# Optimization experiments

Measured on AMD Instinct MI355X. Metric: run time of the kernel, lower is better.

The kernel has to match this reference:

```python
import jax, jax.numpy as jnp
import numpy as np

EDGES = [(5, 7), (7, 9), (6, 8), (8, 10), (5, 6), (5, 11), (6, 12), (11, 12),
         (11, 13), (13, 15), (12, 14), (14, 16), (0, 5), (0, 6)]
N_NODES = 17

def _build_norm_adj():
    # aggregated[dst] += h[src] for both directions; then divide by clamped in-degree.
    A = np.zeros((N_NODES, N_NODES), dtype=np.float32)
    for s, d in EDGES:
        A[d, s] += 1.0
        A[s, d] += 1.0
    deg = np.clip(A.sum(axis=1, keepdims=True), 1.0, None)
    return jnp.asarray(A / deg)  # (17, 17)

_A_NORM = _build_norm_adj()

def _bn17(x, gamma, beta, eps=1e-5):
    # BatchNorm1d(17) on (B, 17, D): stats over batch and feature dims per node channel.
    mean = x.mean(axis=(0, 2), keepdims=True)
    var = x.var(axis=(0, 2), keepdims=True)  # biased, matching torch training mode
    return gamma[None, :, None] * (x - mean) * jax.lax.rsqrt(var + eps) + beta[None, :, None]

def setup_inputs() -> dict:
    key = jax.random.key(0)
    ks = jax.random.split(key, 8)
    B, H, E = 65536, 64, 128
    s = 0.1
    return {
        "x": jax.random.normal(ks[0], (B, N_NODES, 2), jnp.float32),
        "W_enc": jax.random.normal(ks[1], (2, H), jnp.float32) * s,
        "b_enc": jnp.zeros((H,), jnp.float32),
        "W_gc1": jax.random.normal(ks[2], (H, H), jnp.float32) * s,
        "b_gc1": jnp.zeros((H,), jnp.float32),
        "W_gc2": jax.random.normal(ks[3], (H, H), jnp.float32) * s,
        "b_gc2": jnp.zeros((H,), jnp.float32),
        "gamma1": jnp.ones((N_NODES,), jnp.float32),
        "beta1": jnp.zeros((N_NODES,), jnp.float32),
        "gamma2": jnp.ones((N_NODES,), jnp.float32),
        "beta2": jnp.zeros((N_NODES,), jnp.float32),
        "W_p1": jax.random.normal(ks[4], (N_NODES * H, 256), jnp.float32) * s,
        "b_p1": jnp.zeros((256,), jnp.float32),
        "W_p2": jax.random.normal(ks[5], (256, E), jnp.float32) * s,
        "b_p2": jnp.zeros((E,), jnp.float32),
    }

def reference(x, W_enc, b_enc, W_gc1, b_gc1, W_gc2, b_gc2,
              gamma1, beta1, gamma2, beta2, W_p1, b_p1, W_p2, b_p2):
    B = x.shape[0]
    # node encoder (dropout = identity at inference)
    h = jax.nn.relu(jnp.einsum('bnc,cd->bnd', x, W_enc) + b_enc)
    # graph conv 1: normalized neighbor mean via fixed adjacency
    h_agg = jnp.einsum('ij,bjd->bid', _A_NORM, h)
    h = _bn17(h + h_agg, gamma1, beta1)
    h = jax.nn.relu(jnp.einsum('bnd,de->bne', h, W_gc1) + b_gc1)
    # graph conv 2
    h_agg = jnp.einsum('ij,bjd->bid', _A_NORM, h)
    h = _bn17(h + h_agg, gamma2, beta2)
    h = jax.nn.relu(jnp.einsum('bnd,de->bne', h, W_gc2) + b_gc2)
    # pool MLP (dropout = identity)
    pooled = h.reshape(B, -1)  # (B, 17*64)
    z = jax.nn.relu(pooled @ W_p1 + b_p1)
    emb = z @ W_p2 + b_p2
    # L2 normalize (torch F.normalize eps=1e-12)
    norm = jnp.sqrt(jnp.sum(emb * emb, axis=1, keepdims=True))
    return emb / jnp.maximum(norm, 1e-12)
```

## Files before the change

kernel.cpp:

```cpp
#include <hip/hip_runtime.h>
#include <hip/hip_bf16.h>

typedef unsigned int  uint32;
typedef unsigned short ushort16;

#define B_TOTAL 65536
#define NN 17

typedef __bf16 bf16x8 __attribute__((ext_vector_type(8)));
typedef float  f32x4  __attribute__((ext_vector_type(4)));

static constexpr int   CNT[NN]    = {2,0,0,0,0,4,4,2,2,1,1,3,3,2,2,1,1};
static constexpr int   NBR[NN][4] = {
  {5,6,0,0},{0,0,0,0},{0,0,0,0},{0,0,0,0},{0,0,0,0},
  {7,6,11,0},{8,5,12,0},{5,9,0,0},{6,10,0,0},{7,0,0,0},{8,0,0,0},
  {5,12,13,0},{6,11,14,0},{11,15,0,0},{12,16,0,0},{13,0,0,0},{14,0,0,0}};
static constexpr float INVDEG[NN] = {0.5f,0.f,0.f,0.f,0.f,0.25f,0.25f,0.5f,0.5f,1.f,1.f,
  0.33333333333333333f,0.33333333333333333f,0.5f,0.5f,1.f,1.f};

#define S_BYTES   ((size_t)B_TOTAL * 1088 * 2)
#define STATS_OFF S_BYTES
#define W1_OFF    (STATS_OFF + 40960)
#define W2_OFF    (W1_OFF + (size_t)278528*2)
#define WGT_OFF   (W2_OFF + (size_t)65536)


__device__ inline ushort16 f2bfu(float f){
  union { __hip_bfloat16 h; ushort16 u; } c; c.h = __float2bfloat16(f); return c.u;
}

__device__ inline f32x4 MFMA(bf16x8 a, bf16x8 b, f32x4 c){
  return __builtin_amdgcn_mfma_f32_16x16x32_bf16(a, b, c, 0, 0, 0);
}

__device__ inline void gload_lds16(const void* g, void* l){
  __builtin_amdgcn_global_load_lds(
      (const __attribute__((address_space(1))) unsigned int*)g,
      (__attribute__((address_space(3))) unsigned int*)l, 16, 0, 0);
}

__device__ inline void enc_agg(const float* __restrict__ xb,
                               float we0, float we1, float be, float* s1){
  float h[NN];
  #pragma unroll
  for (int n = 0; n < NN; ++n)
    h[n] = fmaxf(fmaf(xb[2*n], we0, fmaf(xb[2*n+1], we1, be)), 0.f);
  #pragma unroll
  for (int n = 0; n < NN; ++n){
    float a = 0.f;
    #pragma unroll
    for (int j = 0; j < 4; ++j) if (j < CNT[n]) a += h[NBR[n][j]];
    s1[n] = fmaf(INVDEG[n], a, h[n]);
  }
}

__device__ inline void reduce_stats(float* sA, float* qA,
                                    float* __restrict__ gSum, float* __restrict__ gSq){
  int t = threadIdx.x;
  #pragma unroll
  for (int n = 0; n < NN; ++n){
    float s = sA[n], q = qA[n];
    #pragma unroll
    for (int off = 32; off > 0; off >>= 1){
      s += __shfl_down(s, off, 64);
      q += __shfl_down(q, off, 64);
    }
    sA[n] = s; qA[n] = q;
  }
  __shared__ float shS[NN], shQ[NN];
  if (t < NN){ shS[t] = 0.f; shQ[t] = 0.f; }
  __syncthreads();
  if ((t & 63) == 0){
    #pragma unroll
    for (int n = 0; n < NN; ++n){ atomicAdd(&shS[n], sA[n]); atomicAdd(&shQ[n], qA[n]); }
  }
  __syncthreads();
  if (t < NN){ atomicAdd(&gSum[t], shS[t]); atomicAdd(&gSq[t], shQ[t]); }
}

__device__ inline void mfma_stats(const char* hsm, float* sred, int t,
                                  float* __restrict__ gSum, float* __restrict__ gSq){
  const int w4 = t >> 6, lo = t & 15, q = (t >> 4) & 3;
  bf16x8 one;
  { union { ushort16 u[8]; bf16x8 v; } c;
    #pragma unroll
    for (int i = 0; i < 8; ++i) c.u[i] = 0x3F80;
    one = c.v; }
  #pragma unroll
  for (int i = 0; i < 5; ++i){
    int mt = w4 + i*4;
    if (mt < 17){
      f32x4 d0 = (f32x4)0.f, d1 = (f32x4)0.f;
      #pragma unroll
      for (int s = 0; s < 2; ++s){
        int r = mt*16 + lo;
        bf16x8 a = *(const bf16x8*)(hsm + ((r*128 + s*64 + q*16) ^ ((r & 7) << 4)));
        d0 = MFMA(a, one, d0);
        d1 = MFMA(a, a, d1);
      }
      if (lo == 0){
        #pragma unroll
        for (int j = 0; j < 4; ++j) sred[mt*16 + q*4 + j] = d0[j];
      }
      if ((lo >> 2) == q) sred[272 + mt*16 + lo] = d1[lo & 3];
    }
  }
  __syncthreads();
  if (t < NN){
    float s = 0.f, qq = 0.f;
    #pragma unroll
    for (int bl = 0; bl < 16; ++bl){
      s  += sred[t + 17*bl];
      qq += sred[272 + t + 17*bl];
    }
    atomicAdd(&gSum[t], s);
    atomicAdd(&gSq[t], qq);
  }
}

__global__ __launch_bounds__(256) void k_prep(const float* __restrict__ Wp1,
                                              const float* __restrict__ Wp2,
                                              const float* __restrict__ Wg1,
                                              const float* __restrict__ Wg2,
                                              ushort16* __restrict__ W1T,
                                              ushort16* __restrict__ W2T,
                                              ushort16* __restrict__ WGT,
                                              float* __restrict__ colsum2){
  int g = blockIdx.x * 256 + threadIdx.x;
  if (g < 278528){
    int n = g / 1088, k = g - n*1088;
    W1T[g] = f2bfu(Wp1[(size_t)k*256 + n]);
  } else if (g < 311296){
    int h = g - 278528;
    int e = h >> 8, k = h & 255;
    W2T[h] = f2bfu(Wp2[(size_t)k*128 + e]);
  } else if (g < 327680){
    int h = g - 311296;
    int sel = h >> 12;
    int idx = h & 4095;
    int e = idx >> 6, d = idx & 63;
    const float* Wsrc = (sel < 2) ? Wg1 : Wg2;
    float v = Wsrc[d*64 + e];
    __hip_bfloat16 hi = __float2bfloat16(v);
    if (sel & 1){
      float rem = v - __bfloat162float(hi);
      WGT[h] = f2bfu(rem);
    } else {
      WGT[h] = f2bfu(v);
    }
  } else {
    int e = g - 327680;
    if (e < 64){
      float cs = 0.f;
      for (int d = 0; d < 64; ++d){
        float v = Wg2[d*64 + e];
        float hi = __bfloat162float(__float2bfloat16(v));
        float lo = __bfloat162float(__float2bfloat16(v - hi));
        cs += hi + lo;
      }
      colsum2[e] = cs;
    }
  }
}

__global__ void k_sh(const float* __restrict__ shift2, const float* __restrict__ colsum2,
                     const float* __restrict__ bg2, float* __restrict__ SH){
  int n = blockIdx.x, e = threadIdx.x;
  SH[n*64 + e] = fmaf(shift2[n], colsum2[e], bg2[e]);
}

__global__ __launch_bounds__(256,4) void k_stats1(const float* __restrict__ x,
    const float* __restrict__ W_enc, const float* __restrict__ b_enc,
    float* __restrict__ gSum, float* __restrict__ gSq){
  __shared__ __align__(16) float xs[1088];
  int t = threadIdx.x, e = t & 63, lb = t >> 6;
  float we0 = W_enc[e], we1 = W_enc[64 + e], be = b_enc[e];
  const float4* xg = (const float4*)(x + (size_t)blockIdx.x*1088);
  ((float4*)xs)[t] = xg[t];
  if (t < 16) ((float4*)xs)[256 + t] = xg[256 + t];
  float sA[NN], qA[NN];
  #pragma unroll
  for (int n = 0; n < NN; ++n){ sA[n] = 0.f; qA[n] = 0.f; }
  __syncthreads();
  for (int it = 0; it < 8; ++it){
    float s1[NN];
    enc_agg(xs + (it*4 + lb)*34, we0, we1, be, s1);
    #pragma unroll
    for (int n = 0; n < NN; ++n){ sA[n] += s1[n]; qA[n] += s1[n]*s1[n]; }
  }
  int slot = (blockIdx.x & 31) * 32;
  reduce_stats(sA, qA, gSum + slot, gSq + slot);
}

__global__ void k_finalize(const float* __restrict__ gSum, const float* __restrict__ gSq,
                           const float* __restrict__ gamma, const float* __restrict__ beta,
                           float* __restrict__ scale, float* __restrict__ shift){
  int n = threadIdx.x;
  if (n < NN){
    float s = 0.f, qq = 0.f;
    for (int sl = 0; sl < 32; ++sl){ s += gSum[sl*32 + n]; qq += gSq[sl*32 + n]; }
    const float invC = 1.0f / (float)((size_t)B_TOTAL * 64);
    float mean = s * invC;
    float var  = qq * invC - mean*mean;
    float istd = rsqrtf(var + 1e-5f);
    float sc   = gamma[n] * istd;
    scale[n] = sc;
    shift[n] = fmaf(-mean, sc, beta[n]);
  }
}

__global__ __launch_bounds__(256,4) void k_gc1(const float* __restrict__ x,
    const float* __restrict__ W_enc, const float* __restrict__ b_enc,
    const float* __restrict__ bg,
    const float* __restrict__ scale, const float* __restrict__ shift,
    const __hip_bfloat16* __restrict__ Whi, const __hip_bfloat16* __restrict__ Wlo,
    __hip_bfloat16* __restrict__ S, float* __restrict__ gSum, float* __restrict__ gSq){
  __shared__ __align__(16) char hsm[272*128];
  __shared__ float sred[544];
  __shared__ __align__(16) float xs[544];
  __shared__ float sc_s[NN], sf_s[NN];
  const int t = threadIdx.x, e = t & 63, lb = t >> 6;
  const int w4 = t >> 6, lo = t & 15, q = (t >> 4) & 3;
  if (t < NN){ sc_s[t] = scale[t]; sf_s[t] = shift[t]; }
  if (t < 136) ((float4*)xs)[t] = ((const float4*)(x + (size_t)blockIdx.x*544))[t];
  float we0 = W_enc[e], we1 = W_enc[64 + e], be = b_enc[e];
  __syncthreads();

  for (int it = 0; it < 4; ++it){
    int bl = it*4 + lb;
    float s1[NN];
    enc_agg(xs + bl*34, we0, we1, be, s1);
    #pragma unroll
    for (int n = 0; n < NN; ++n){
      int row = bl*17 + n;
      int byt = (row*128 + 2*e) ^ ((row & 7) << 4);
      *(__hip_bfloat16*)(hsm + byt) = __float2bfloat16(fmaf(s1[n], sc_s[n], sf_s[n]));
    }
  }
  __syncthreads();

  const char* WhiB = (const char*)Whi;
  const char* WloB = (const char*)Wlo;
  f32x4 acc[5][4];
  #pragma unroll
  for (int i = 0; i < 5; ++i)
    #pragma unroll
    for (int et = 0; et < 4; ++et) acc[i][et] = (f32x4)0.f;
  #pragma unroll
  for (int et = 0; et < 4; ++et){
    int col = et*16 + lo;
    bf16x8 wh0 = *(const bf16x8*)(WhiB + col*128 +      q*16);
    bf16x8 wh1 = *(const bf16x8*)(WhiB + col*128 + 64 + q*16);
    bf16x8 wl0 = *(const bf16x8*)(WloB + col*128 +      q*16);
    bf16x8 wl1 = *(const bf16x8*)(WloB + col*128 + 64 + q*16);
    #pragma unroll
    for (int i = 0; i < 5; ++i){
      int mt = w4 + i*4;
      if (mt < 17){
        int r = mt*16 + lo;
        int base = r*128, sw = (r & 7) << 4;
        bf16x8 a0 = *(const bf16x8*)(hsm + ((base +      q*16) ^ sw));
        bf16x8 a1 = *(const bf16x8*)(hsm + ((base + 64 + q*16) ^ sw));
        acc[i][et] = MFMA(a0, wh0, acc[i][et]);
        acc[i][et] = MFMA(a1, wh1, acc[i][et]);
        acc[i][et] = MFMA(a0, wl0, acc[i][et]);
        acc[i][et] = MFMA(a1, wl1, acc[i][et]);
      }
    }
  }
  float bgv[4];
  #pragma unroll
  for (int et = 0; et < 4; ++et) bgv[et] = bg[et*16 + lo];
  __syncthreads();

  #pragma unroll
  for (int i = 0; i < 5; ++i){
    int mt = w4 + i*4;
    if (mt < 17){
      #pragma unroll
      for (int et = 0; et < 4; ++et){
        #pragma unroll
        for (int j = 0; j < 4; ++j){
          int row = mt*16 + q*4 + j;
          float h2 = fmaxf(acc[i][et][j] + bgv[et], 0.f);
          int byt = (row*128 + (et*16 + lo)*2) ^ ((row & 7) << 4);
          *(__hip_bfloat16*)(hsm + byt) = __float2bfloat16(h2);
        }
      }
    }
  }
  __syncthreads();

  for (int it = 0; it < 4; ++it){
    int bl = it*4 + lb;
    int row0 = bl*17;
    float h2v[NN];
    #pragma unroll
    for (int n = 0; n < NN; ++n){
      int row = row0 + n;
      h2v[n] = __bfloat162float(*(const __hip_bfloat16*)(hsm + ((row*128 + 2*e) ^ ((row & 7) << 4))));
    }
    #pragma unroll
    for (int n = 0; n < NN; ++n){
      float agg = 0.f;
      #pragma unroll
      for (int j = 0; j < 4; ++j) if (j < CNT[n]) agg += h2v[NBR[n][j]];
      float s2 = fmaf(INVDEG[n], agg, h2v[n]);
      int row = row0 + n;
      *(__hip_bfloat16*)(hsm + ((row*128 + 2*e) ^ ((row & 7) << 4))) = __float2bfloat16(s2);
    }
  }
  __syncthreads();

  int slot = (blockIdx.x & 31) * 32;
  mfma_stats(hsm, sred, t, gSum + slot, gSq + slot);

  const size_t gbase = (size_t)blockIdx.x * 34816;
  char* Sc = (char*)S;
  #pragma unroll
  for (int k = 0; k < 9; ++k){
    int g = t + k*256;
    if (g < 2176){
      int row = g >> 3;
      uint4 v = *(const uint4*)(hsm + ((g*16) ^ ((row & 7) << 4)));
      *(uint4*)(Sc + gbase + (size_t)g*16) = v;
    }
  }
}

__global__ __launch_bounds__(256,2) void k_back(
    const __hip_bfloat16* __restrict__ S,
    const ushort16* __restrict__ W1T, const float* __restrict__ b_p1,
    const ushort16* __restrict__ W2T, const float* __restrict__ b_p2,
    const __hip_bfloat16* __restrict__ WG2,
    const float* __restrict__ scale2, const float* __restrict__ SH,
    float* __restrict__ out){
  __shared__ __align__(16) char smem[65536];
  const int t = threadIdx.x;
  const int L = t & 63, w = t >> 6;
  const int lo = L & 15, q = L >> 4;
  const int wsw = ((lo >> 1) & 3) << 4;
  const size_t b0 = (size_t)blockIdx.x * 128;
  const char* Sb  = (const char*)S;
  const char* W1b = (const char*)W1T;
  const char* W2b = (const char*)W2T;
  const char* Wgb = (const char*)WG2;

  f32x4 acc[16][2];
  #pragma unroll
  for (int nt = 0; nt < 16; ++nt){ acc[nt][0] = (f32x4)0.f; acc[nt][1] = (f32x4)0.f; }

  bf16x8 wg[4][4];
  #pragma unroll
  for (int et = 0; et < 4; ++et){
    const char* A = Wgb + (et*16 + lo)*128 + q*16;
    wg[et][0] = *(const bf16x8*)(A);
    wg[et][1] = *(const bf16x8*)(A + 64);
    wg[et][2] = *(const bf16x8*)(A + 8192);
    wg[et][3] = *(const bf16x8*)(A + 8192 + 64);
  }

  const int csw = (((t & 3) * 16) ^ (((t >> 3) & 3) << 4));
  auto stageW = [&](int ks, int buf){
    size_t kb = (size_t)ks * 64;
    char* ldsbase = smem + 32768 + buf*16384 + w*1024;
    gload_lds16(W1b + (size_t)((  0 + t) >> 2)*2176 + kb + csw, ldsbase);
    gload_lds16(W1b + (size_t)((256 + t) >> 2)*2176 + kb + csw, ldsbase + 4096);
    gload_lds16(W1b + (size_t)((512 + t) >> 2)*2176 + kb + csw, ldsbase + 8192);
    gload_lds16(W1b + (size_t)((768 + t) >> 2)*2176 + kb + csw, ldsbase + 12288);
  };

  uint4 br[4];
  auto loadS2 = [&](int n){
    const char* base = Sb + (b0 + (size_t)(w*32 + lo))*2176 + n*128 + q*16;
    br[0] = *(const uint4*)(base);
    br[1] = *(const uint4*)(base + 64);
    br[2] = *(const uint4*)(base + 16*2176);
    br[3] = *(const uint4*)(base + 16*2176 + 64);
  };
  auto gc2w = [&](int n){
    char* Pb = smem + (n & 1)*16384;
    float sc = scale2[n];
    #pragma unroll
    for (int bt = 0; bt < 2; ++bt){
      f32x4 g[4];
      #pragma unroll
      for (int et = 0; et < 4; ++et) g[et] = (f32x4)0.f;
      union { uint4 u; bf16x8 v; } c0, c1;
      c0.u = br[bt*2]; c1.u = br[bt*2 + 1];
      #pragma unroll
      for (int et = 0; et < 4; ++et){
        g[et] = MFMA(wg[et][0], c0.v, g[et]);
        g[et] = MFMA(wg[et][2], c0.v, g[et]);
        g[et] = MFMA(wg[et][1], c1.v, g[et]);
        g[et] = MFMA(wg[et][3], c1.v, g[et]);
      }
      int b = w*32 + bt*16 + lo;
      #pragma unroll
      for (int et = 0; et < 4; ++et){
        float4 sh4 = *(const float4*)&SH[n*64 + et*16 + q*4];
        float v0 = fmaxf(fmaf(sc, g[et].x, sh4.x), 0.f);
        float v1 = fmaxf(fmaf(sc, g[et].y, sh4.y), 0.f);
        float v2 = fmaxf(fmaf(sc, g[et].z, sh4.z), 0.f);
        float v3 = fmaxf(fmaf(sc, g[et].w, sh4.w), 0.f);
        uint32 u0 = (uint32)f2bfu(v0) | ((uint32)f2bfu(v1) << 16);
        uint32 u1 = (uint32)f2bfu(v2) | ((uint32)f2bfu(v3) << 16);
        int byt = (b*128 + (et*16 + q*4)*2) ^ ((b & 7) << 4);
        *(uint2*)(Pb + byt) = make_uint2(u0, u1);
      }
    }
  };

  loadS2(0);
  gc2w(0);
  stageW(0, 0);
  __syncthreads();

  #pragma unroll 1
  for (int ks = 0; ks < 34; ++ks){
    const int cur = ks & 1, n = ks >> 1, half = ks & 1;
    if (ks < 33) stageW(ks + 1, cur ^ 1);
    if (half == 0 && n < 16) loadS2(n + 1);
    const char* Pb = smem + (n & 1)*16384;
    const char* Wb = smem + 32768 + (cur ? 16384 : 0);
    int r0 = w*32 + lo, r1 = w*32 + 16 + lo;
    bf16x8 pf0 = *(const bf16x8*)(Pb + ((r0*128 + half*64 + q*16) ^ ((r0 & 7) << 4)));
    bf16x8 pf1 = *(const bf16x8*)(Pb + ((r1*128 + half*64 + q*16) ^ ((r1 & 7) << 4)));
    #pragma unroll
    for (int nt = 0; nt < 16; ++nt){
      bf16x8 wf = *(const bf16x8*)(Wb + (nt*16 + lo)*64 + (q*16 ^ wsw));
      acc[nt][0] = MFMA(wf, pf0, acc[nt][0]);
      acc[nt][1] = MFMA(wf, pf1, acc[nt][1]);
    }
    if (half == 1 && n < 16) gc2w(n + 1);
    __syncthreads();
  }

  #pragma unroll
  for (int nt = 0; nt < 16; ++nt){
    float4 bias = *(const float4*)&b_p1[nt*16 + q*4];
    #pragma unroll
    for (int bt = 0; bt < 2; ++bt){
      int b = w*32 + bt*16 + lo;
      f32x4 v = acc[nt][bt];
      float z0 = fmaxf(v.x + bias.x, 0.f), z1 = fmaxf(v.y + bias.y, 0.f);
      float z2 = fmaxf(v.z + bias.z, 0.f), z3 = fmaxf(v.w + bias.w, 0.f);
      uint32 lo32 = (uint32)f2bfu(z0) | ((uint32)f2bfu(z1) << 16);
      uint32 hi32 = (uint32)f2bfu(z2) | ((uint32)f2bfu(z3) << 16);
      int nbyte = (nt*16 + q*4) * 2;
      int addr = b*512 + (nbyte ^ ((b & 7) << 4));
      *(uint2*)(smem + addr) = make_uint2(lo32, hi32);
    }
  }
  __syncthreads();

  f32x4 acc2[8][2];
  #pragma unroll
  for (int et = 0; et < 8; ++et){ acc2[et][0] = (f32x4)0.f; acc2[et][1] = (f32x4)0.f; }
  #pragma unroll 1
  for (int ks = 0; ks < 8; ++ks){
    bf16x8 zf0, zf1;
    {
      int b = w*32 + lo;
      int kb = ks*64 + q*16;
      zf0 = *(const bf16x8*)(smem + b*512 + (kb ^ ((b & 7) << 4)));
      b = w*32 + 16 + lo;
      zf1 = *(const bf16x8*)(smem + b*512 + (kb ^ ((b & 7) << 4)));
    }
    #pragma unroll
    for (int et = 0; et < 8; ++et){
      bf16x8 wf = *(const bf16x8*)(W2b + (et*16 + lo)*512 + ks*64 + q*16);
      acc2[et][0] = MFMA(wf, zf0, acc2[et][0]);
      acc2[et][1] = MFMA(wf, zf1, acc2[et][1]);
    }
  }

  #pragma unroll
  for (int bt = 0; bt < 2; ++bt){
    int b = w*32 + bt*16 + lo;
    float4 vv[8];
    float ss = 0.f;
    #pragma unroll
    for (int et = 0; et < 8; ++et){
      float4 bias = *(const float4*)&b_p2[et*16 + q*4];
      f32x4 a = bt ? acc2[et][1] : acc2[et][0];
      vv[et].x = a.x + bias.x; vv[et].y = a.y + bias.y;
      vv[et].z = a.z + bias.z; vv[et].w = a.w + bias.w;
      ss += vv[et].x*vv[et].x + vv[et].y*vv[et].y + vv[et].z*vv[et].z + vv[et].w*vv[et].w;
    }
    ss += __shfl_xor(ss, 16, 64);
    ss += __shfl_xor(ss, 32, 64);
    float inv = 1.0f / fmaxf(sqrtf(ss), 1e-12f);
    float* op = out + (b0 + b)*128;
    #pragma unroll
    for (int et = 0; et < 8; ++et){
      float4 o; o.x = vv[et].x*inv; o.y = vv[et].y*inv; o.z = vv[et].z*inv; o.w = vv[et].w*inv;
      *(float4*)(op + et*16 + q*4) = o;
    }
  }
}

extern "C" void kernel_launch(void* const* d_in, const int* in_sizes, int n_in,
                              void* d_out, int out_size, void* d_ws, size_t ws_size,
                              hipStream_t stream) {
  const float* x     = (const float*)d_in[0];
  const float* W_enc = (const float*)d_in[1];
  const float* b_enc = (const float*)d_in[2];
  const float* W_gc1 = (const float*)d_in[3];
  const float* b_gc1 = (const float*)d_in[4];
  const float* W_gc2 = (const float*)d_in[5];
  const float* b_gc2 = (const float*)d_in[6];
  const float* gamma1= (const float*)d_in[7];
  const float* beta1 = (const float*)d_in[8];
  const float* gamma2= (const float*)d_in[9];
  const float* beta2 = (const float*)d_in[10];
  const float* W_p1  = (const float*)d_in[11];
  const float* b_p1  = (const float*)d_in[12];
  const float* W_p2  = (const float*)d_in[13];
  const float* b_p2  = (const float*)d_in[14];
  float* out = (float*)d_out;

  char* ws = (char*)d_ws;
  __hip_bfloat16* S = (__hip_bfloat16*)ws;
  float*    stats = (float*)(ws + STATS_OFF);
  ushort16* W1T   = (ushort16*)(ws + W1_OFF);
  ushort16* W2T   = (ushort16*)(ws + W2_OFF);
  __hip_bfloat16* WGT = (__hip_bfloat16*)(ws + WGT_OFF);

  (void)hipMemsetAsync(stats, 0, 16384, stream);

  k_prep<<<1281, 256, 0, stream>>>(W_p1, W_p2, W_gc1, W_gc2, W1T, W2T,
                                   (ushort16*)WGT, stats + 4224);
  k_stats1<<<2048, 256, 0, stream>>>(x, W_enc, b_enc, stats + 0, stats + 1024);
  k_finalize<<<1, 32, 0, stream>>>(stats + 0, stats + 1024, gamma1, beta1,
                                   stats + 4096, stats + 4128);
  k_gc1<<<4096, 256, 0, stream>>>(x, W_enc, b_enc, b_gc1,
                                  stats + 4096, stats + 4128,
                                  WGT, WGT + 4096,
                                  S, stats + 2048, stats + 3072);
  k_finalize<<<1, 32, 0, stream>>>(stats + 2048, stats + 3072, gamma2, beta2,
                                   stats + 4160, stats + 4192);
  k_sh<<<17, 64, 0, stream>>>(stats + 4192, stats + 4224, b_gc2, stats + 4288);
  k_back<<<512, 256, 0, stream>>>(S, W1T, b_p1, W2T, b_p2,
                                  WGT + 8192, stats + 4160, stats + 4288, out);
}
```

Measured before the change: 325.9 us.

## Fuse second-layer aggregation, BN stats and store into one vectorized pass

The end of k_gc1 changes. Before, it did the neighbor aggregation per element, then a barrier, an MFMA-based stats pass and a separate copy-out. Now each thread takes a 16-byte octet of a row, reads the neighbor octets from LDS through a packed lookup table, computes the aggregate, writes the bf16 result straight to global memory, and accumulates sum and sum-of-squares with shuffles and LDS atomics. This removes one LDS round trip, two barriers and the MFMA stats, at the cost of more LDS atomics, a loop that is no longer unrolled, and integer-division arithmetic per slot. enc_agg also now reads the input as float2.

```diff
diff --git a/kernel.cpp b/kernel.cpp
--- a/kernel.cpp
+++ b/kernel.cpp
@@ -39,12 +39,19 @@
       (__attribute__((address_space(3))) unsigned int*)l, 16, 0, 0);
 }
 
-__device__ inline void enc_agg(const float* __restrict__ xb,
+__device__ inline void w8(uint4 u, float* f){
+  f[0]=__uint_as_float(u.x<<16); f[1]=__uint_as_float(u.x&0xFFFF0000u);
+  f[2]=__uint_as_float(u.y<<16); f[3]=__uint_as_float(u.y&0xFFFF0000u);
+  f[4]=__uint_as_float(u.z<<16); f[5]=__uint_as_float(u.z&0xFFFF0000u);
+  f[6]=__uint_as_float(u.w<<16); f[7]=__uint_as_float(u.w&0xFFFF0000u);
+}
+
+__device__ inline void enc_agg(const float2* __restrict__ xb,
                                float we0, float we1, float be, float* s1){
   float h[NN];
   #pragma unroll
   for (int n = 0; n < NN; ++n)
-    h[n] = fmaxf(fmaf(xb[2*n], we0, fmaf(xb[2*n+1], we1, be)), 0.f);
+    h[n] = fmaxf(fmaf(xb[n].x, we0, fmaf(xb[n].y, we1, be)), 0.f);
   #pragma unroll
   for (int n = 0; n < NN; ++n){
     float a = 0.f;
@@ -76,46 +83,6 @@
   }
   __syncthreads();
   if (t < NN){ atomicAdd(&gSum[t], shS[t]); atomicAdd(&gSq[t], shQ[t]); }
-}
-
-__device__ inline void mfma_stats(const char* hsm, float* sred, int t,
-                                  float* __restrict__ gSum, float* __restrict__ gSq){
-  const int w4 = t >> 6, lo = t & 15, q = (t >> 4) & 3;
-  bf16x8 one;
-  { union { ushort16 u[8]; bf16x8 v; } c;
-    #pragma unroll
-    for (int i = 0; i < 8; ++i) c.u[i] = 0x3F80;
-    one = c.v; }
-  #pragma unroll
-  for (int i = 0; i < 5; ++i){
-    int mt = w4 + i*4;
-    if (mt < 17){
-      f32x4 d0 = (f32x4)0.f, d1 = (f32x4)0.f;
-      #pragma unroll
-      for (int s = 0; s < 2; ++s){
-        int r = mt*16 + lo;
-        bf16x8 a = *(const bf16x8*)(hsm + ((r*128 + s*64 + q*16) ^ ((r & 7) << 4)));
-        d0 = MFMA(a, one, d0);
-        d1 = MFMA(a, a, d1);
-      }
-      if (lo == 0){
-        #pragma unroll
-        for (int j = 0; j < 4; ++j) sred[mt*16 + q*4 + j] = d0[j];
-      }
-      if ((lo >> 2) == q) sred[272 + mt*16 + lo] = d1[lo & 3];
-    }
-  }
-  __syncthreads();
-  if (t < NN){
-    float s = 0.f, qq = 0.f;
-    #pragma unroll
-    for (int bl = 0; bl < 16; ++bl){
-      s  += sred[t + 17*bl];
-      qq += sred[272 + t + 17*bl];
-    }
-    atomicAdd(&gSum[t], s);
-    atomicAdd(&gSq[t], qq);
-  }
 }
 
 __global__ __launch_bounds__(256) void k_prep(const float* __restrict__ Wp1,
@@ -184,7 +151,7 @@
   __syncthreads();
   for (int it = 0; it < 8; ++it){
     float s1[NN];
-    enc_agg(xs + (it*4 + lb)*34, we0, we1, be, s1);
+    enc_agg((const float2*)(xs + (it*4 + lb)*34), we0, we1, be, s1);
     #pragma unroll
     for (int n = 0; n < NN; ++n){ sA[n] += s1[n]; qA[n] += s1[n]*s1[n]; }
   }
@@ -216,12 +183,19 @@
     const __hip_bfloat16* __restrict__ Whi, const __hip_bfloat16* __restrict__ Wlo,
     __hip_bfloat16* __restrict__ S, float* __restrict__ gSum, float* __restrict__ gSq){
   __shared__ __align__(16) char hsm[272*128];
-  __shared__ float sred[544];
   __shared__ __align__(16) float xs[544];
   __shared__ float sc_s[NN], sf_s[NN];
+  __shared__ uint32 lutP[NN];
+  __shared__ float lutI[NN], shS[NN], shQ[NN];
   const int t = threadIdx.x, e = t & 63, lb = t >> 6;
   const int w4 = t >> 6, lo = t & 15, q = (t >> 4) & 3;
-  if (t < NN){ sc_s[t] = scale[t]; sf_s[t] = shift[t]; }
+  if (t < NN){
+    sc_s[t] = scale[t]; sf_s[t] = shift[t];
+    lutP[t] = (uint32)CNT[t] | ((uint32)NBR[t][0]<<3) | ((uint32)NBR[t][1]<<8)
+            | ((uint32)NBR[t][2]<<13) | ((uint32)NBR[t][3]<<18);
+    lutI[t] = INVDEG[t];
+    shS[t] = 0.f; shQ[t] = 0.f;
+  }
   if (t < 136) ((float4*)xs)[t] = ((const float4*)(x + (size_t)blockIdx.x*544))[t];
   float we0 = W_enc[e], we1 = W_enc[64 + e], be = b_enc[e];
   __syncthreads();
@@ -229,7 +203,7 @@
   for (int it = 0; it < 4; ++it){
     int bl = it*4 + lb;
     float s1[NN];
-    enc_agg(xs + bl*34, we0, we1, be, s1);
+    enc_agg((const float2*)(xs + bl*34), we0, we1, be, s1);
     #pragma unroll
     for (int n = 0; n < NN; ++n){
       int row = bl*17 + n;
@@ -291,40 +265,56 @@
   }
   __syncthreads();
 
-  for (int it = 0; it < 4; ++it){
-    int bl = it*4 + lb;
-    int row0 = bl*17;
-    float h2v[NN];
-    #pragma unroll
-    for (int n = 0; n < NN; ++n){
-      int row = row0 + n;
-      h2v[n] = __bfloat162float(*(const __hip_bfloat16*)(hsm + ((row*128 + 2*e) ^ ((row & 7) << 4))));
-    }
-    #pragma unroll
-    for (int n = 0; n < NN; ++n){
-      float agg = 0.f;
-      #pragma unroll
-      for (int j = 0; j < 4; ++j) if (j < CNT[n]) agg += h2v[NBR[n][j]];
-      float s2 = fmaf(INVDEG[n], agg, h2v[n]);
-      int row = row0 + n;
-      *(__hip_bfloat16*)(hsm + ((row*128 + 2*e) ^ ((row & 7) << 4))) = __float2bfloat16(s2);
-    }
-  }
-  __syncthreads();
-
-  int slot = (blockIdx.x & 31) * 32;
-  mfma_stats(hsm, sred, t, gSum + slot, gSq + slot);
-
   const size_t gbase = (size_t)blockIdx.x * 34816;
   char* Sc = (char*)S;
-  #pragma unroll
+  #pragma unroll 1
   for (int k = 0; k < 9; ++k){
-    int g = t + k*256;
-    if (g < 2176){
-      int row = g >> 3;
-      uint4 v = *(const uint4*)(hsm + ((g*16) ^ ((row & 7) << 4)));
-      *(uint4*)(Sc + gbase + (size_t)g*16) = v;
-    }
+    int slot = t + k*256;
+    if (slot < 2176){
+      int r = slot >> 3, oct = slot & 7;
+      int n = r - 17*((r*61681)>>20);
+      int rb = r - n;
+      uint32 pk = lutP[n];
+      float inv = lutI[n];
+      uint4 uo = *(const uint4*)(hsm + ((r*128 + oct*16) ^ ((r & 7) << 4)));
+      float own[8]; w8(uo, own);
+      float agg[8];
+      #pragma unroll
+      for (int i = 0; i < 8; ++i) agg[i] = 0.f;
+      int cnt = pk & 7;
+      #pragma unroll
+      for (int j = 0; j < 4; ++j){
+        if (j < cnt){
+          int nb = rb + (int)((pk >> (3 + 5*j)) & 31);
+          uint4 un = *(const uint4*)(hsm + ((nb*128 + oct*16) ^ ((nb & 7) << 4)));
+          float nf[8]; w8(un, nf);
+          #pragma unroll
+          for (int i = 0; i < 8; ++i) agg[i] += nf[i];
+        }
+      }
+      uint32 ou[4];
+      float s = 0.f, qq = 0.f;
+      #pragma unroll
+      for (int i2 = 0; i2 < 4; ++i2){
+        float a  = fmaf(inv, agg[2*i2],   own[2*i2]);
+        float b2 = fmaf(inv, agg[2*i2+1], own[2*i2+1]);
+        ushort16 ua = f2bfu(a), ub = f2bfu(b2);
+        ou[i2] = (uint32)ua | ((uint32)ub << 16);
+        float ra  = __uint_as_float((uint32)ua << 16);
+        float rb2 = __uint_as_float((uint32)ub << 16);
+        s += ra + rb2; qq += ra*ra + rb2*rb2;
+      }
+      *(uint4*)(Sc + gbase + (size_t)r*128 + oct*16) = make_uint4(ou[0],ou[1],ou[2],ou[3]);
+      s  += __shfl_down(s, 4, 64);  s  += __shfl_down(s, 2, 64);  s  += __shfl_down(s, 1, 64);
+      qq += __shfl_down(qq, 4, 64); qq += __shfl_down(qq, 2, 64); qq += __shfl_down(qq, 1, 64);
+      if ((t & 7) == 0){ atomicAdd(&shS[n], s); atomicAdd(&shQ[n], qq); }
+    }
+  }
+  __syncthreads();
+  if (t < NN){
+    int slot2 = (blockIdx.x & 31) * 32;
+    atomicAdd(&gSum[slot2 + t], shS[t]);
+    atomicAdd(&gSq[slot2 + t], shQ[t]);
   }
 }
 
```

Result: slower. 339.0 us (+4.0%).

## Cut k_back LDS to 48KB for three blocks per CU, single-buffer W1

Applied to the files above, without the earlier changes.

Shrinks k_back's shared memory from 64KB to 48KB and raises launch bounds to allow three blocks per CU. The W1 tile is now single-buffered, with staging moved after compute behind an extra barrier. The second MLP stage is split into two 64-row chunks so the z buffer fits in the smaller LDS. The goal is more resident waves to hide latency, at the cost of losing W1 prefetch overlap, adding barriers, and tighter register limits.

```diff
diff --git a/kernel.cpp b/kernel.cpp
--- a/kernel.cpp
+++ b/kernel.cpp
@@ -328,14 +328,14 @@
   }
 }
 
-__global__ __launch_bounds__(256,2) void k_back(
+__global__ __launch_bounds__(256,3) void k_back(
     const __hip_bfloat16* __restrict__ S,
     const ushort16* __restrict__ W1T, const float* __restrict__ b_p1,
     const ushort16* __restrict__ W2T, const float* __restrict__ b_p2,
     const __hip_bfloat16* __restrict__ WG2,
     const float* __restrict__ scale2, const float* __restrict__ SH,
     float* __restrict__ out){
-  __shared__ __align__(16) char smem[65536];
+  __shared__ __align__(16) char smem[49152];
   const int t = threadIdx.x;
   const int L = t & 63, w = t >> 6;
   const int lo = L & 15, q = L >> 4;
@@ -361,9 +361,9 @@
   }
 
   const int csw = (((t & 3) * 16) ^ (((t >> 3) & 3) << 4));
-  auto stageW = [&](int ks, int buf){
+  auto stageW = [&](int ks){
     size_t kb = (size_t)ks * 64;
-    char* ldsbase = smem + 32768 + buf*16384 + w*1024;
+    char* ldsbase = smem + 32768 + w*1024;
     gload_lds16(W1b + (size_t)((  0 + t) >> 2)*2176 + kb + csw, ldsbase);
     gload_lds16(W1b + (size_t)((256 + t) >> 2)*2176 + kb + csw, ldsbase + 4096);
     gload_lds16(W1b + (size_t)((512 + t) >> 2)*2176 + kb + csw, ldsbase + 8192);
@@ -413,16 +413,15 @@
 
   loadS2(0);
   gc2w(0);
-  stageW(0, 0);
+  stageW(0);
   __syncthreads();
 
   #pragma unroll 1
   for (int ks = 0; ks < 34; ++ks){
-    const int cur = ks & 1, n = ks >> 1, half = ks & 1;
-    if (ks < 33) stageW(ks + 1, cur ^ 1);
+    const int n = ks >> 1, half = ks & 1;
     if (half == 0 && n < 16) loadS2(n + 1);
     const char* Pb = smem + (n & 1)*16384;
-    const char* Wb = smem + 32768 + (cur ? 16384 : 0);
+    const char* Wb = smem + 32768;
     int r0 = w*32 + lo, r1 = w*32 + 16 + lo;
     bf16x8 pf0 = *(const bf16x8*)(Pb + ((r0*128 + half*64 + q*16) ^ ((r0 & 7) << 4)));
     bf16x8 pf1 = *(const bf16x8*)(Pb + ((r1*128 + half*64 + q*16) ^ ((r1 & 7) << 4)));
@@ -434,69 +433,68 @@
     }
     if (half == 1 && n < 16) gc2w(n + 1);
     __syncthreads();
-  }
-
-  #pragma unroll
-  for (int nt = 0; nt < 16; ++nt){
-    float4 bias = *(const float4*)&b_p1[nt*16 + q*4];
-    #pragma unroll
-    for (int bt = 0; bt < 2; ++bt){
-      int b = w*32 + bt*16 + lo;
-      f32x4 v = acc[nt][bt];
-      float z0 = fmaxf(v.x + bias.x, 0.f), z1 = fmaxf(v.y + bias.y, 0.f);
-      float z2 = fmaxf(v.z + bias.z, 0.f), z3 = fmaxf(v.w + bias.w, 0.f);
-      uint32 lo32 = (uint32)f2bfu(z0) | ((uint32)f2bfu(z1) << 16);
-      uint32 hi32 = (uint32)f2bfu(z2) | ((uint32)f2bfu(z3) << 16);
-      int nbyte = (nt*16 + q*4) * 2;
-      int addr = b*512 + (nbyte ^ ((b & 7) << 4));
-      *(uint2*)(smem + addr) = make_uint2(lo32, hi32);
-    }
-  }
-  __syncthreads();
-
-  f32x4 acc2[8][2];
-  #pragma unroll
-  for (int et = 0; et < 8; ++et){ acc2[et][0] = (f32x4)0.f; acc2[et][1] = (f32x4)0.f; }
+    if (ks < 33){
+      stageW(ks + 1);
+      __syncthreads();
+    }
+  }
+
   #pragma unroll 1
-  for (int ks = 0; ks < 8; ++ks){
-    bf16x8 zf0, zf1;
-    {
-      int b = w*32 + lo;
-      int kb = ks*64 + q*16;
-      zf0 = *(const bf16x8*)(smem + b*512 + (kb ^ ((b & 7) << 4)));
-      b = w*32 + 16 + lo;
-      zf1 = *(const bf16x8*)(smem + b*512 + (kb ^ ((b & 7) << 4)));
-    }
-    #pragma unroll
-    for (int et = 0; et < 8; ++et){
-      bf16x8 wf = *(const bf16x8*)(W2b + (et*16 + lo)*512 + ks*64 + q*16);
-      acc2[et][0] = MFMA(wf, zf0, acc2[et][0]);
-      acc2[et][1] = MFMA(wf, zf1, acc2[et][1]);
-    }
-  }
-
-  #pragma unroll
-  for (int bt = 0; bt < 2; ++bt){
-    int b = w*32 + bt*16 + lo;
+  for (int c = 0; c < 2; ++c){
+    if ((w >> 1) == c){
+      int j = w & 1;
+      #pragma unroll
+      for (int nt = 0; nt < 16; ++nt){
+        float4 bias = *(const float4*)&b_p1[nt*16 + q*4];
+        #pragma unroll
+        for (int bt = 0; bt < 2; ++bt){
+          int lr = j*32 + bt*16 + lo;
+          f32x4 v = acc[nt][bt];
+          float z0 = fmaxf(v.x + bias.x, 0.f), z1 = fmaxf(v.y + bias.y, 0.f);
+          float z2 = fmaxf(v.z + bias.z, 0.f), z3 = fmaxf(v.w + bias.w, 0.f);
+          uint32 lo32 = (uint32)f2bfu(z0) | ((uint32)f2bfu(z1) << 16);
+          uint32 hi32 = (uint32)f2bfu(z2) | ((uint32)f2bfu(z3) << 16);
+          int nbyte = (nt*16 + q*4) * 2;
+          int addr = lr*512 + (nbyte ^ ((lr & 7) << 4));
+          *(uint2*)(smem + addr) = make_uint2(lo32, hi32);
+        }
+      }
+    }
+    __syncthreads();
+
+    f32x4 acc2[8];
+    #pragma unroll
+    for (int et = 0; et < 8; ++et) acc2[et] = (f32x4)0.f;
+    #pragma unroll
+    for (int ks2 = 0; ks2 < 8; ++ks2){
+      int lr = w*16 + lo;
+      bf16x8 zf = *(const bf16x8*)(smem + lr*512 + ((ks2*64 + q*16) ^ ((lr & 7) << 4)));
+      #pragma unroll
+      for (int et = 0; et < 8; ++et){
+        bf16x8 wf2 = *(const bf16x8*)(W2b + (et*16 + lo)*512 + ks2*64 + q*16);
+        acc2[et] = MFMA(wf2, zf, acc2[et]);
+      }
+    }
+
     float4 vv[8];
     float ss = 0.f;
     #pragma unroll
     for (int et = 0; et < 8; ++et){
       float4 bias = *(const float4*)&b_p2[et*16 + q*4];
-      f32x4 a = bt ? acc2[et][1] : acc2[et][0];
-      vv[et].x = a.x + bias.x; vv[et].y = a.y + bias.y;
-      vv[et].z = a.z + bias.z; vv[et].w = a.w + bias.w;
+      vv[et].x = acc2[et].x + bias.x; vv[et].y = acc2[et].y + bias.y;
+      vv[et].z = acc2[et].z + bias.z; vv[et].w = acc2[et].w + bias.w;
       ss += vv[et].x*vv[et].x + vv[et].y*vv[et].y + vv[et].z*vv[et].z + vv[et].w*vv[et].w;
     }
     ss += __shfl_xor(ss, 16, 64);
     ss += __shfl_xor(ss, 32, 64);
     float inv = 1.0f / fmaxf(sqrtf(ss), 1e-12f);
-    float* op = out + (b0 + b)*128;
+    float* op = out + (b0 + c*64 + w*16 + lo)*128;
     #pragma unroll
     for (int et = 0; et < 8; ++et){
       float4 o; o.x = vv[et].x*inv; o.y = vv[et].y*inv; o.z = vv[et].z*inv; o.w = vv[et].w*inv;
       *(float4*)(op + et*16 + q*4) = o;
     }
+    __syncthreads();
   }
 }
 
```

Result: slower. 913.4 us (+180.2%).
